# Kernel tuning notes

Hardware: AMD Instinct MI355X
Metric: run time of the kernel (lower is better)

Reference implementation:

```python
import jax, jax.numpy as jnp
import numpy as np

F_IN = 512
F_OUT = 512
HEADS = 8  # all heads share the same weights in the original module
NEG_SLOPE = 0.01  # nn.LeakyReLU default
MASK_VAL = -1.0e10


def setup_inputs() -> dict:
    key = jax.random.key(0)
    ks = jax.random.split(key, 6)
    B, N = 8, 2048
    X_input = jax.random.normal(ks[0], (B, N, F_IN), dtype=jnp.float32)
    u = jax.random.uniform(ks[1], (B, N, N), dtype=jnp.float32)
    A_input = jnp.maximum((u < 0.02).astype(jnp.float32), jnp.eye(N, dtype=jnp.float32)[None])
    # learned params (nn.Linear stores W as [out,in]; we use [in,out] with x @ W)
    Wk = jax.random.normal(ks[2], (F_IN, F_OUT), dtype=jnp.float32) / np.sqrt(F_IN).astype(np.float32)
    bk = jnp.zeros((F_OUT,), dtype=jnp.float32)
    ws = jax.random.normal(ks[3], (F_OUT,), dtype=jnp.float32) / np.sqrt(F_OUT).astype(np.float32)
    bs = jnp.zeros((), dtype=jnp.float32)
    wn = jax.random.normal(ks[4], (F_OUT,), dtype=jnp.float32) / np.sqrt(F_OUT).astype(np.float32)
    bn = jnp.zeros((), dtype=jnp.float32)
    return {"X_input": X_input, "A_input": A_input, "Wk": Wk, "bk": bk,
            "ws": ws, "bs": bs, "wn": wn, "bn": bn}


def reference(X_input, A_input, Wk, bk, ws, bs, wn, bn):
    # shared projection (identical across all heads in the original loop)
    feat = jnp.einsum('bnf,fg->bng', X_input, Wk) + bk          # [B,N,F_]
    a_self = jnp.einsum('bng,g->bn', feat, ws) + bs             # [B,N]
    a_neigh = jnp.einsum('bng,g->bn', feat, wn) + bn            # [B,N]
    # torch.bmm([B,N,1],[B,1,N]) -> multiplicative outer product score
    att = jax.nn.leaky_relu(a_self[:, :, None] * a_neigh[:, None, :], NEG_SLOPE)
    att = att + MASK_VAL * (1.0 - A_input)                      # [B,N,N]
    p = jax.nn.softmax(att, axis=-1)
    nf = jnp.einsum('bij,bjg->big', p, feat)                    # [B,N,F_]
    # concat of HEADS identical head outputs, then tanh
    out = jnp.tanh(jnp.concatenate([nf] * HEADS, axis=-1))      # [B,N,HEADS*F_]
    return out
```

## Files before the change

### kernel.cpp

```cpp
#include <hip/hip_runtime.h>

#define NEG_SLOPE 0.01f
#define B_ 8
#define N_ 2048
#define F_ 512

typedef unsigned short u16;
typedef __attribute__((ext_vector_type(8))) unsigned short u16x8;
typedef __attribute__((ext_vector_type(8))) _Float16 f16x8;
typedef __attribute__((ext_vector_type(4))) float f32x4;

__device__ __forceinline__ f32x4 mfma16f(u16x8 a, u16x8 b, f32x4 c) {
    return __builtin_amdgcn_mfma_f32_16x16x32_f16(
        __builtin_bit_cast(f16x8, a), __builtin_bit_cast(f16x8, b), c, 0, 0, 0);
}

__device__ __forceinline__ void load_lds16(const void* g, void* l) {
    __builtin_amdgcn_global_load_lds(
        (__attribute__((address_space(1))) void*)(void*)g,
        (__attribute__((address_space(3))) void*)l, 16, 0, 0);
}

__global__ __launch_bounds__(256) void prep_all(const float* __restrict__ Wk,
                                                const float* __restrict__ bk,
                                                const float* __restrict__ ws,
                                                const float* __restrict__ bs,
                                                const float* __restrict__ wn,
                                                const float* __restrict__ bn,
                                                u16* __restrict__ Wf,
                                                float* __restrict__ ws2,
                                                float* __restrict__ wn2,
                                                float* __restrict__ csn) {
    const int bid = blockIdx.x, t = threadIdx.x;
    if (bid < 1024) {
        const int id = bid * 256 + t;
        const int k = id & 511, n = id >> 9;
        ((_Float16*)Wf)[id] = (_Float16)Wk[k * 512 + n];
        return;
    }
    const int lane = t & 63, w = t >> 6;
    if (bid >= 1280) {
        if (w == 0) {
            const int sel = bid - 1280;
            const float* vec = sel ? wn : ws;
            const float4 b0 = *(const float4*)(bk + lane * 8);
            const float4 b1 = *(const float4*)(bk + lane * 8 + 4);
            const float4 v0 = *(const float4*)(vec + lane * 8);
            const float4 v1 = *(const float4*)(vec + lane * 8 + 4);
            float d = b0.x * v0.x + b0.y * v0.y + b0.z * v0.z + b0.w * v0.w +
                      b1.x * v1.x + b1.y * v1.y + b1.z * v1.z + b1.w * v1.w;
#pragma unroll
            for (int m = 32; m; m >>= 1) d += __shfl_xor(d, m);
            if (lane == 0) csn[sel] = d + (sel ? bn[0] : bs[0]);
        }
        return;
    }
    const int W = (bid - 1024) * 4 + w;
    const int k = W & 511;
    const float* vec = (W < 512) ? ws : wn;
    const float4 w0 = *(const float4*)(Wk + (size_t)k * 512 + lane * 8);
    const float4 w1 = *(const float4*)(Wk + (size_t)k * 512 + lane * 8 + 4);
    const float4 v0 = *(const float4*)(vec + lane * 8);
    const float4 v1 = *(const float4*)(vec + lane * 8 + 4);
    float d = w0.x * v0.x + w0.y * v0.y + w0.z * v0.z + w0.w * v0.w +
              w1.x * v1.x + w1.y * v1.y + w1.z * v1.z + w1.w * v1.w;
#pragma unroll
    for (int m = 32; m; m >>= 1) d += __shfl_xor(d, m);
    if (lane == 0) ((W < 512) ? ws2 : wn2)[k] = d;
}

__global__ __launch_bounds__(256) void gemm_feat(const float* __restrict__ X,
                                                 const u16* __restrict__ Wf,
                                                 const float* __restrict__ bk,
                                                 u16* __restrict__ feat) {
    __shared__ u16 Af[128 * 64];
    __shared__ u16 Bf[128 * 64];
    const int t = threadIdx.x;
    const int lane = t & 63;
    const int w = t >> 6;
    const int bid = blockIdx.x;
    const int tm = (bid & 7) * 16 + (bid >> 5);
    const int tn = (bid >> 3) & 3;
    const int wr = w >> 1, wc = w & 1;

    f32x4 acc[4][4];
#pragma unroll
    for (int m = 0; m < 4; ++m)
#pragma unroll
        for (int n = 0; n < 4; ++n) acc[m][n] = {0.f, 0.f, 0.f, 0.f};

    const int lrow = lane >> 3;
    const int scol = ((lane & 7) ^ lrow) * 8;
    const u16* Bbase = Wf + ((size_t)(tn * 128 + w * 8 + lrow)) * 512 + scol;
    u16* BfW = Bf + (w * 8) * 64;

    const int arow = t >> 3;
    const int akk = (t & 7) * 8;
    const float* Abase = X + ((size_t)(tm * 128 + arow)) * 512 + akk;
    u16* AfW = Af + arow * 64 + (akk ^ ((arow & 7) * 8));

    for (int k0 = 0; k0 < 512; k0 += 64) {
#pragma unroll
        for (int iss = 0; iss < 4; ++iss)
            load_lds16(Bbase + (size_t)(iss * 32) * 512 + k0, BfW + iss * 32 * 64);
#pragma unroll
        for (int p = 0; p < 4; ++p) {
            const float4 x0 = *(const float4*)(Abase + (size_t)(p * 32) * 512 + k0);
            const float4 x1 = *(const float4*)(Abase + (size_t)(p * 32) * 512 + k0 + 4);
            const float xv[8] = {x0.x, x0.y, x0.z, x0.w, x1.x, x1.y, x1.z, x1.w};
            u16x8 hv;
#pragma unroll
            for (int e = 0; e < 8; ++e)
                hv[e] = __builtin_bit_cast(u16, (_Float16)xv[e]);
            *(u16x8*)(AfW + p * 32 * 64) = hv;
        }
        __syncthreads();
        const int swz = (lane & 7) * 8;
#pragma unroll
        for (int kk = 0; kk < 64; kk += 32) {
            u16x8 af[4], bf[4];
            const int aoff = (kk + (lane >> 4) * 8) ^ swz;
#pragma unroll
            for (int m = 0; m < 4; ++m)
                af[m] = *(const u16x8*)(Af + (wr * 64 + m * 16 + (lane & 15)) * 64 + aoff);
#pragma unroll
            for (int n = 0; n < 4; ++n)
                bf[n] = *(const u16x8*)(Bf + (wc * 64 + n * 16 + (lane & 15)) * 64 + aoff);
#pragma unroll
            for (int m = 0; m < 4; ++m)
#pragma unroll
                for (int n = 0; n < 4; ++n)
                    acc[m][n] = mfma16f(af[m], bf[n], acc[m][n]);
        }
        __syncthreads();
    }

    const int crow0 = tm * 128 + wr * 64;
    const int ccol0 = tn * 128 + wc * 64;
    _Float16* feat16 = (_Float16*)feat;
#pragma unroll
    for (int n = 0; n < 4; ++n) {
        const int gc = ccol0 + n * 16 + (lane & 15);
        const float bkv = bk[gc];
#pragma unroll
        for (int m = 0; m < 4; ++m) {
            const int gr = crow0 + m * 16 + (lane >> 4) * 4;
#pragma unroll
            for (int r = 0; r < 4; ++r)
                feat16[(size_t)(gr + r) * 512 + gc] = (_Float16)(acc[m][n][r] + bkv);
        }
    }
}

__global__ __launch_bounds__(256) void dots_x(const float* __restrict__ X,
                                              const float* __restrict__ ws2,
                                              const float* __restrict__ wn2,
                                              const float* __restrict__ csn,
                                              float* __restrict__ a_self,
                                              float* __restrict__ a_neigh) {
    const int t = threadIdx.x, lane = t & 63, w = t >> 6;
    const int row = blockIdx.x * 4 + w;
    const float4 f0 = *(const float4*)(X + (size_t)row * 512 + lane * 8);
    const float4 f1 = *(const float4*)(X + (size_t)row * 512 + lane * 8 + 4);
    const float fv[8] = {f0.x, f0.y, f0.z, f0.w, f1.x, f1.y, f1.z, f1.w};
    const float4 sa = *(const float4*)(ws2 + lane * 8);
    const float4 sb = *(const float4*)(ws2 + lane * 8 + 4);
    const float4 na = *(const float4*)(wn2 + lane * 8);
    const float4 nb = *(const float4*)(wn2 + lane * 8 + 4);
    float ds = fv[0] * sa.x + fv[1] * sa.y + fv[2] * sa.z + fv[3] * sa.w +
               fv[4] * sb.x + fv[5] * sb.y + fv[6] * sb.z + fv[7] * sb.w;
    float dn = fv[0] * na.x + fv[1] * na.y + fv[2] * na.z + fv[3] * na.w +
               fv[4] * nb.x + fv[5] * nb.y + fv[6] * nb.z + fv[7] * nb.w;
#pragma unroll
    for (int m = 32; m; m >>= 1) {
        ds += __shfl_xor(ds, m);
        dn += __shfl_xor(dn, m);
    }
    if (lane == 0) {
        a_self[row] = ds + csn[0];
        a_neigh[row] = dn + csn[1];
    }
}

__global__ __launch_bounds__(256) void compact_rows(const float* __restrict__ A,
                                                    const float* __restrict__ a_self,
                                                    const float* __restrict__ a_neigh,
                                                    float2* __restrict__ list,
                                                    int* __restrict__ cnt_arr) {
    const int bid = blockIdx.x;
    const int t = threadIdx.x, lane = t & 63, w = t >> 6;
    const int row = bid * 4 + w;
    const int b = row >> 11;

    const float asi = a_self[row];
    const float4* Arow4 = (const float4*)(A + (size_t)row * N_);
    const float4* An4   = (const float4*)(a_neigh + (size_t)b * N_);

    float sv[32];
    unsigned selbits = 0;
    float mloc = -3.0e38f;
#pragma unroll
    for (int c = 0; c < 8; ++c) {
        const float4 a  = Arow4[c * 64 + lane];
        const float4 an = An4[c * 64 + lane];
        const float avi[4] = {a.x, a.y, a.z, a.w};
        const float ani[4] = {an.x, an.y, an.z, an.w};
#pragma unroll
        for (int i = 0; i < 4; ++i) {
            float s = asi * ani[i];
            s = s > 0.f ? s : NEG_SLOPE * s;
            sv[c * 4 + i] = s;
            if (avi[i] != 0.f) {
                selbits |= 1u << (c * 4 + i);
                mloc = fmaxf(mloc, s);
            }
        }
    }
    float mx = mloc;
#pragma unroll
    for (int m = 32; m; m >>= 1) mx = fmaxf(mx, __shfl_xor(mx, m));

    float lsum = 0.f;
    {
        unsigned mbits = selbits;
        while (mbits) {
            const int e = __builtin_ctz(mbits);
            mbits &= mbits - 1;
            const float p = __expf(sv[e] - mx);
            sv[e] = p;
            lsum += p;
        }
    }
    float tot = lsum;
#pragma unroll
    for (int m = 32; m; m >>= 1) tot += __shfl_xor(tot, m);
    const float inv = 1.f / tot;

    const int cntl = __popc(selbits);
    int v = cntl;
#pragma unroll
    for (int off = 1; off < 64; off <<= 1) {
        const int u = __shfl_up(v, off);
        if (lane >= off) v += u;
    }
    if (lane == 63) cnt_arr[row] = v;
    int pos = v - cntl;

    float2* lr = list + (size_t)row * 128;
    {
        unsigned mbits = selbits;
        while (mbits) {
            const int e = __builtin_ctz(mbits);
            mbits &= mbits - 1;
            const int j = (e >> 2) * 256 + lane * 4 + (e & 3);
            lr[pos] = make_float2(sv[e] * inv, (float)j);
            ++pos;
        }
    }
}

__global__ __launch_bounds__(256) void gather_rows(const float2* __restrict__ list,
                                                   const int* __restrict__ cnt_arr,
                                                   const u16* __restrict__ feat,
                                                   float* __restrict__ out) {
    const int bid = blockIdx.x;
    const int t = threadIdx.x, lane = t & 63, w = t >> 6;
    const int b = bid & 7;
    const int row = b * N_ + (bid >> 3) * 4 + w;

    const int cnt = cnt_arr[row];
    const float2* lr = list + (size_t)row * 128;
    const float2 e0 = lr[lane];
    const float2 e1 = lr[64 + lane];

    const u16* frow = feat + (size_t)b * N_ * F_ + lane * 8;
    float acc[8] = {0.f, 0.f, 0.f, 0.f, 0.f, 0.f, 0.f, 0.f};

    const int c0 = cnt < 64 ? cnt : 64;
    int k = 0;
    for (; k + 4 <= c0; k += 4) {
        const float p0 = __shfl(e0.x, k),     j0 = __shfl(e0.y, k);
        const float p1 = __shfl(e0.x, k + 1), j1 = __shfl(e0.y, k + 1);
        const float p2 = __shfl(e0.x, k + 2), j2 = __shfl(e0.y, k + 2);
        const float p3 = __shfl(e0.x, k + 3), j3 = __shfl(e0.y, k + 3);
        const f16x8 v0 = *(const f16x8*)(frow + (size_t)(int)j0 * F_);
        const f16x8 v1 = *(const f16x8*)(frow + (size_t)(int)j1 * F_);
        const f16x8 v2 = *(const f16x8*)(frow + (size_t)(int)j2 * F_);
        const f16x8 v3 = *(const f16x8*)(frow + (size_t)(int)j3 * F_);
#pragma unroll
        for (int i = 0; i < 8; ++i)
            acc[i] += (p0 * (float)v0[i] + p1 * (float)v1[i]) +
                      (p2 * (float)v2[i] + p3 * (float)v3[i]);
    }
    for (; k < c0; ++k) {
        const float p0 = __shfl(e0.x, k), j0 = __shfl(e0.y, k);
        const f16x8 v0 = *(const f16x8*)(frow + (size_t)(int)j0 * F_);
#pragma unroll
        for (int i = 0; i < 8; ++i) acc[i] += p0 * (float)v0[i];
    }
    for (k = 64; k < cnt; ++k) {
        const float p0 = __shfl(e1.x, k - 64), j0 = __shfl(e1.y, k - 64);
        const f16x8 v0 = *(const f16x8*)(frow + (size_t)(int)j0 * F_);
#pragma unroll
        for (int i = 0; i < 8; ++i) acc[i] += p0 * (float)v0[i];
    }

    float o[8];
#pragma unroll
    for (int i = 0; i < 8; ++i) o[i] = tanhf(acc[i]);
    const float4 o0 = {o[0], o[1], o[2], o[3]};
    const float4 o1 = {o[4], o[5], o[6], o[7]};
    float* obase = out + (size_t)row * (8 * F_) + lane * 8;
#pragma unroll
    for (int h = 0; h < 8; ++h) {
        *(float4*)(obase + h * F_)     = o0;
        *(float4*)(obase + h * F_ + 4) = o1;
    }
}

extern "C" void kernel_launch(void* const* d_in, const int* in_sizes, int n_in,
                              void* d_out, int out_size, void* d_ws, size_t ws_size,
                              hipStream_t stream) {
    const float* X  = (const float*)d_in[0];
    const float* A  = (const float*)d_in[1];
    const float* Wk = (const float*)d_in[2];
    const float* bk = (const float*)d_in[3];
    const float* ws = (const float*)d_in[4];
    const float* bs = (const float*)d_in[5];
    const float* wn = (const float*)d_in[6];
    const float* bn = (const float*)d_in[7];
    float* out = (float*)d_out;

    char* wsb = (char*)d_ws;
    u16*   feat    = (u16*)(wsb);
    u16*   Wf      = (u16*)(wsb + 16777216);
    float* a_self  = (float*)(wsb + 17301504);
    float* a_neigh = (float*)(wsb + 17367040);
    float* ws2     = (float*)(wsb + 17432576);
    float* wn2     = (float*)(wsb + 17434624);
    float* csn     = (float*)(wsb + 17436672);
    int*   cnt_arr = (int*)(wsb + 17440768);
    float2* list   = (float2*)(wsb + 17825792);

    prep_all     <<<dim3(1282), dim3(256), 0, stream>>>(Wk, bk, ws, bs, wn, bn, Wf, ws2, wn2, csn);
    dots_x       <<<dim3(4096), dim3(256), 0, stream>>>(X, ws2, wn2, csn, a_self, a_neigh);
    compact_rows <<<dim3(4096), dim3(256), 0, stream>>>(A, a_self, a_neigh, list, cnt_arr);
    gemm_feat    <<<dim3(512),  dim3(256), 0, stream>>>(X, Wf, bk, feat);
    gather_rows  <<<dim3(4096), dim3(256), 0, stream>>>(list, cnt_arr, feat, out);
}
```

Before: 155.8 us.

## Use nontemporal loads/stores, LDS edge list, 8-wide gather, recompute scores

The adjacency read in compact_rows and the list read and output write in gather_rows now use nontemporal loads and stores. The edge list is staged through LDS so the gather loop can be unrolled 8-wide without shuffles. compact_rows no longer keeps a 32-float score array in registers and instead recomputes scores from a_neigh, which lowers register pressure at the cost of extra loads and exps. The weight-transpose prep now reads coalesced and writes strided.

After: 147.0 us. 5.6% less time.

```diff
diff --git a/kernel.cpp b/kernel.cpp
--- a/kernel.cpp
+++ b/kernel.cpp
@@ -34,8 +34,8 @@
     const int bid = blockIdx.x, t = threadIdx.x;
     if (bid < 1024) {
         const int id = bid * 256 + t;
-        const int k = id & 511, n = id >> 9;
-        ((_Float16*)Wf)[id] = (_Float16)Wk[k * 512 + n];
+        const int k = id >> 9, n = id & 511;
+        ((_Float16*)Wf)[(size_t)n * 512 + k] = (_Float16)Wk[id];
         return;
     }
     const int lane = t & 63, w = t >> 6;
@@ -193,15 +193,15 @@
     const int b = row >> 11;
 
     const float asi = a_self[row];
-    const float4* Arow4 = (const float4*)(A + (size_t)row * N_);
-    const float4* An4   = (const float4*)(a_neigh + (size_t)b * N_);
-
-    float sv[32];
+    const f32x4* Arow4 = (const f32x4*)(A + (size_t)row * N_);
+    const float* anb   = a_neigh + (size_t)b * N_;
+    const float4* An4  = (const float4*)anb;
+
     unsigned selbits = 0;
     float mloc = -3.0e38f;
 #pragma unroll
     for (int c = 0; c < 8; ++c) {
-        const float4 a  = Arow4[c * 64 + lane];
+        const f32x4 a  = __builtin_nontemporal_load(&Arow4[c * 64 + lane]);
         const float4 an = An4[c * 64 + lane];
         const float avi[4] = {a.x, a.y, a.z, a.w};
         const float ani[4] = {an.x, an.y, an.z, an.w};
@@ -209,7 +209,6 @@
         for (int i = 0; i < 4; ++i) {
             float s = asi * ani[i];
             s = s > 0.f ? s : NEG_SLOPE * s;
-            sv[c * 4 + i] = s;
             if (avi[i] != 0.f) {
                 selbits |= 1u << (c * 4 + i);
                 mloc = fmaxf(mloc, s);
@@ -226,9 +225,10 @@
         while (mbits) {
             const int e = __builtin_ctz(mbits);
             mbits &= mbits - 1;
-            const float p = __expf(sv[e] - mx);
-            sv[e] = p;
-            lsum += p;
+            const int j = (e >> 2) * 256 + lane * 4 + (e & 3);
+            float s = asi * anb[j];
+            s = s > 0.f ? s : NEG_SLOPE * s;
+            lsum += __expf(s - mx);
         }
     }
     float tot = lsum;
@@ -243,7 +243,8 @@
         const int u = __shfl_up(v, off);
         if (lane >= off) v += u;
     }
-    if (lane == 63) cnt_arr[row] = v;
+    const int total = __shfl(v, 63);
+    if (lane == 0) cnt_arr[row] = total;
     int pos = v - cntl;
 
     float2* lr = list + (size_t)row * 128;
@@ -253,7 +254,9 @@
             const int e = __builtin_ctz(mbits);
             mbits &= mbits - 1;
             const int j = (e >> 2) * 256 + lane * 4 + (e & 3);
-            lr[pos] = make_float2(sv[e] * inv, (float)j);
+            float s = asi * anb[j];
+            s = s > 0.f ? s : NEG_SLOPE * s;
+            lr[pos] = make_float2(__expf(s - mx) * inv, (float)j);
             ++pos;
         }
     }
@@ -263,58 +266,69 @@
                                                    const int* __restrict__ cnt_arr,
                                                    const u16* __restrict__ feat,
                                                    float* __restrict__ out) {
+    __shared__ float2 sc[4][128];
     const int bid = blockIdx.x;
     const int t = threadIdx.x, lane = t & 63, w = t >> 6;
     const int b = bid & 7;
     const int row = b * N_ + (bid >> 3) * 4 + w;
 
     const int cnt = cnt_arr[row];
-    const float2* lr = list + (size_t)row * 128;
-    const float2 e0 = lr[lane];
-    const float2 e1 = lr[64 + lane];
+    {
+        const f32x4 le = __builtin_nontemporal_load(
+            (const f32x4*)(list + (size_t)row * 128) + lane);
+        *((f32x4*)sc[w] + lane) = le;
+    }
+    float2* scw = sc[w];
 
     const u16* frow = feat + (size_t)b * N_ * F_ + lane * 8;
     float acc[8] = {0.f, 0.f, 0.f, 0.f, 0.f, 0.f, 0.f, 0.f};
-
-    const int c0 = cnt < 64 ? cnt : 64;
     int k = 0;
-    for (; k + 4 <= c0; k += 4) {
-        const float p0 = __shfl(e0.x, k),     j0 = __shfl(e0.y, k);
-        const float p1 = __shfl(e0.x, k + 1), j1 = __shfl(e0.y, k + 1);
-        const float p2 = __shfl(e0.x, k + 2), j2 = __shfl(e0.y, k + 2);
-        const float p3 = __shfl(e0.x, k + 3), j3 = __shfl(e0.y, k + 3);
-        const f16x8 v0 = *(const f16x8*)(frow + (size_t)(int)j0 * F_);
-        const f16x8 v1 = *(const f16x8*)(frow + (size_t)(int)j1 * F_);
-        const f16x8 v2 = *(const f16x8*)(frow + (size_t)(int)j2 * F_);
-        const f16x8 v3 = *(const f16x8*)(frow + (size_t)(int)j3 * F_);
+    for (; k + 8 <= cnt; k += 8) {
+        const float2 E0 = scw[k],     E1 = scw[k + 1], E2 = scw[k + 2], E3 = scw[k + 3];
+        const float2 E4 = scw[k + 4], E5 = scw[k + 5], E6 = scw[k + 6], E7 = scw[k + 7];
+        const f16x8 v0 = *(const f16x8*)(frow + (size_t)(int)E0.y * F_);
+        const f16x8 v1 = *(const f16x8*)(frow + (size_t)(int)E1.y * F_);
+        const f16x8 v2 = *(const f16x8*)(frow + (size_t)(int)E2.y * F_);
+        const f16x8 v3 = *(const f16x8*)(frow + (size_t)(int)E3.y * F_);
+        const f16x8 v4 = *(const f16x8*)(frow + (size_t)(int)E4.y * F_);
+        const f16x8 v5 = *(const f16x8*)(frow + (size_t)(int)E5.y * F_);
+        const f16x8 v6 = *(const f16x8*)(frow + (size_t)(int)E6.y * F_);
+        const f16x8 v7 = *(const f16x8*)(frow + (size_t)(int)E7.y * F_);
 #pragma unroll
         for (int i = 0; i < 8; ++i)
-            acc[i] += (p0 * (float)v0[i] + p1 * (float)v1[i]) +
-                      (p2 * (float)v2[i] + p3 * (float)v3[i]);
-    }
-    for (; k < c0; ++k) {
-        const float p0 = __shfl(e0.x, k), j0 = __shfl(e0.y, k);
-        const f16x8 v0 = *(const f16x8*)(frow + (size_t)(int)j0 * F_);
-#pragma unroll
-        for (int i = 0; i < 8; ++i) acc[i] += p0 * (float)v0[i];
-    }
-    for (k = 64; k < cnt; ++k) {
-        const float p0 = __shfl(e1.x, k - 64), j0 = __shfl(e1.y, k - 64);
-        const f16x8 v0 = *(const f16x8*)(frow + (size_t)(int)j0 * F_);
-#pragma unroll
-        for (int i = 0; i < 8; ++i) acc[i] += p0 * (float)v0[i];
+            acc[i] += ((E0.x * (float)v0[i] + E1.x * (float)v1[i]) +
+                       (E2.x * (float)v2[i] + E3.x * (float)v3[i])) +
+                      ((E4.x * (float)v4[i] + E5.x * (float)v5[i]) +
+                       (E6.x * (float)v6[i] + E7.x * (float)v7[i]));
+    }
+    for (; k + 4 <= cnt; k += 4) {
+        const float2 E0 = scw[k], E1 = scw[k + 1], E2 = scw[k + 2], E3 = scw[k + 3];
+        const f16x8 v0 = *(const f16x8*)(frow + (size_t)(int)E0.y * F_);
+        const f16x8 v1 = *(const f16x8*)(frow + (size_t)(int)E1.y * F_);
+        const f16x8 v2 = *(const f16x8*)(frow + (size_t)(int)E2.y * F_);
+        const f16x8 v3 = *(const f16x8*)(frow + (size_t)(int)E3.y * F_);
+#pragma unroll
+        for (int i = 0; i < 8; ++i)
+            acc[i] += (E0.x * (float)v0[i] + E1.x * (float)v1[i]) +
+                      (E2.x * (float)v2[i] + E3.x * (float)v3[i]);
+    }
+    for (; k < cnt; ++k) {
+        const float2 E0 = scw[k];
+        const f16x8 v0 = *(const f16x8*)(frow + (size_t)(int)E0.y * F_);
+#pragma unroll
+        for (int i = 0; i < 8; ++i) acc[i] += E0.x * (float)v0[i];
     }
 
     float o[8];
 #pragma unroll
     for (int i = 0; i < 8; ++i) o[i] = tanhf(acc[i]);
-    const float4 o0 = {o[0], o[1], o[2], o[3]};
-    const float4 o1 = {o[4], o[5], o[6], o[7]};
+    const f32x4 o0 = {o[0], o[1], o[2], o[3]};
+    const f32x4 o1 = {o[4], o[5], o[6], o[7]};
     float* obase = out + (size_t)row * (8 * F_) + lane * 8;
 #pragma unroll
     for (int h = 0; h < 8; ++h) {
-        *(float4*)(obase + h * F_)     = o0;
-        *(float4*)(obase + h * F_ + 4) = o1;
+        __builtin_nontemporal_store(o0, (f32x4*)(obase + h * F_));
+        __builtin_nontemporal_store(o1, (f32x4*)(obase + h * F_ + 4));
     }
 }
 
```
